# Optimization experiments

Measured on AMD Instinct MI355X. Metric: run time of the kernel, lower is better.

## Reference

```python
import jax, jax.numpy as jnp
import numpy as np

B, N, S, D = 32, 128, 64, 512
MAX_LEN = 5000


def make_pe(d_model, max_len):
    pos = np.arange(max_len, dtype=np.float32)[:, None]
    div = np.exp(np.arange(0, d_model, 2, dtype=np.float32) * (-np.log(10000.0) / d_model))
    pe = np.zeros((max_len, d_model), dtype=np.float32)
    pe[:, 0::2] = np.sin(pos * div)
    pe[:, 1::2] = np.cos(pos * div)
    return jnp.asarray(pe)


def setup_inputs() -> dict:
    key = jax.random.key(0)
    ks = jax.random.split(key, 16)
    s1 = 1.0 / np.sqrt(D)
    s2 = 1.0 / np.sqrt(2 * D)
    inp = {
        "x": jax.random.normal(ks[0], (B, N), jnp.float32),
        "timesteps": jax.random.randint(ks[1], (B,), 0, 1000),
        "fusion_feat": jax.random.normal(ks[2], (B, D), jnp.float32),
        "tar_image_feat": jax.random.normal(ks[3], (B, N, S, D), jnp.float32),
        "pe": make_pe(D, MAX_LEN),
        # torch Linear weights are [out, in]
        "Wq": jax.random.normal(ks[4], (D, D), jnp.float32) * s1,
        "Wk": jax.random.normal(ks[5], (D, D), jnp.float32) * s1,
        "Wv": jax.random.normal(ks[6], (D, D), jnp.float32) * s1,
        "Wp": jax.random.normal(ks[7], (D, D), jnp.float32) * s1,
        "bp": jnp.zeros((D,), jnp.float32),
        "Wt1": jax.random.normal(ks[8], (D, D), jnp.float32) * s1,
        "bt1": jnp.zeros((D,), jnp.float32),
        "Wt2": jax.random.normal(ks[9], (D, D), jnp.float32) * s1,
        "bt2": jnp.zeros((D,), jnp.float32),
        "Wd1": jax.random.normal(ks[10], (2 * D, 2 * D), jnp.float32) * s2,
        "bd1": jnp.zeros((2 * D,), jnp.float32),
        "Wd2": jax.random.normal(ks[11], (1, 2 * D), jnp.float32) * s2,
        "bd2": jnp.zeros((1,), jnp.float32),
    }
    return inp


def reference(x, timesteps, fusion_feat, tar_image_feat, pe,
              Wq, Wk, Wv, Wp, bp, Wt1, bt1, Wt2, bt2, Wd1, bd1, Wd2, bd2):
    # timestep embedding: pe[timesteps] -> [B, D], then 2-layer SiLU MLP (eval mode: dropout off)
    cond = jax.nn.silu(pe[timesteps] @ Wt1.T + bt1) @ Wt2.T + bt2  # [B, D]

    # similarity argmax over S tokens, then gather best token per (b, n)
    sim = jnp.einsum('bd,bnsd->bns', fusion_feat, tar_image_feat)  # [B, N, S]
    best = jnp.argmax(sim, axis=-1)                                # [B, N]
    tif = jnp.take_along_axis(tar_image_feat, best[:, :, None, None], axis=2)[:, :, 0, :]  # [B, N, D]

    # single-vector attention over N candidates
    q = (fusion_feat + cond) @ Wq.T                  # [B, D]
    k = (tif + cond[:, None, :]) @ Wk.T              # [B, N, D]
    v = (tif + cond[:, None, :]) @ Wv.T              # [B, N, D]
    w = jax.nn.softmax(jnp.einsum('bd,bnd->bn', q, k) + x, axis=-1)  # [B, N]
    new_emb = jnp.einsum('bn,bnd->bd', w, v) @ Wp.T + bp             # [B, D]

    # MLP decode over concat [new_emb (broadcast), tif]
    emb = jnp.concatenate([jnp.broadcast_to(new_emb[:, None, :], tif.shape), tif], axis=-1)  # [B, N, 2D]
    h = jax.nn.relu(emb @ Wd1.T + bd1)
    p = (h @ Wd2.T + bd2)[..., 0] + w                # [B, N]

    # sort descending along N
    return -jnp.sort(-p, axis=1)
```

## Files before the change

kernel.cpp:

```cpp
#include <hip/hip_runtime.h>
#include <hip/hip_bf16.h>
#include <math.h>


#define BB 32
#define NN 128
#define SS 64
#define DD 512

typedef __attribute__((ext_vector_type(8))) short short8;
typedef __attribute__((ext_vector_type(4))) float f32x4;

__device__ __forceinline__ ushort f2bf(float f) {
    unsigned u = __float_as_uint(f);
    unsigned r = (u + 0x7fffu + ((u >> 16) & 1u)) >> 16;
    return (ushort)r;
}

__device__ __forceinline__ void wave_dot512x4(
    const float* __restrict__ w, size_t ldw, float4 xa, float4 xb,
    int lane, float out[4]) {
    float4 ra[4], rb[4];
#pragma unroll
    for (int r = 0; r < 4; ++r) {
        const float4* row = reinterpret_cast<const float4*>(w + (size_t)r * ldw);
        ra[r] = row[lane * 2];
        rb[r] = row[lane * 2 + 1];
    }
#pragma unroll
    for (int r = 0; r < 4; ++r) {
        float s = ra[r].x * xa.x + ra[r].y * xa.y + ra[r].z * xa.z + ra[r].w * xa.w
                + rb[r].x * xb.x + rb[r].y * xb.y + rb[r].z * xb.z + rb[r].w * xb.w;
#pragma unroll
        for (int off = 32; off; off >>= 1) s += __shfl_xor(s, off);
        out[r] = s;
    }
}

__global__ __launch_bounds__(256) void bmv(
    const float* __restrict__ W, int ldw, const float* __restrict__ bias,
    const float* __restrict__ Xa, const float* __restrict__ Xb,
    const int* __restrict__ ts, const float* __restrict__ pe,
    float* __restrict__ Y, int R, int act, int mode) {
    __shared__ __align__(16) float xl[DD];
    int b = blockIdx.y, tid = threadIdx.x, lane = tid & 63, wave = tid >> 6;
    const float* src = (mode == 1) ? (pe + (size_t)ts[b] * DD) : (Xa + (size_t)b * DD);
    if (mode == 2) {
        const float* s2 = Xb + (size_t)b * DD;
        for (int i = tid; i < DD; i += 256) xl[i] = src[i] + s2[i];
    } else {
        for (int i = tid; i < DD; i += 256) xl[i] = src[i];
    }
    __syncthreads();
    float4 xa = reinterpret_cast<const float4*>(xl)[lane * 2];
    float4 xb = reinterpret_cast<const float4*>(xl)[lane * 2 + 1];
    int j0 = blockIdx.x * 16 + wave * 4;
    float s[4];
    wave_dot512x4(W + (size_t)j0 * ldw, ldw, xa, xb, lane, s);
    if (lane < 4) {
        int j = j0 + lane;
        float v = s[lane];
        if (bias) v += bias[j];
        if (act == 1) v = v / (1.f + expf(-v));
        Y[(size_t)b * R + j] = v;
    }
}

__global__ __launch_bounds__(256) void k_qk(
    const float* __restrict__ Wk, const float* __restrict__ q,
    float* __restrict__ qk) {
    __shared__ __align__(16) float ql[DD];
    __shared__ float part[4][64];
    int b = blockIdx.y, c0 = blockIdx.x * 64;
    int tid = threadIdx.x, lane = tid & 63, wave = tid >> 6;
    for (int i = tid; i < DD; i += 256) ql[i] = q[(size_t)b * DD + i];
    __syncthreads();
    float p = 0.f;
    for (int j = wave * 128; j < wave * 128 + 128; ++j)
        p += ql[j] * Wk[(size_t)j * DD + c0 + lane];
    part[wave][lane] = p;
    __syncthreads();
    if (tid < 64)
        qk[(size_t)b * DD + c0 + tid] =
            part[0][tid] + part[1][tid] + part[2][tid] + part[3][tid];
}

__global__ __launch_bounds__(256) void k2_sim(
    const float* __restrict__ fusion, const float* __restrict__ tif,
    const float* __restrict__ x, const float* __restrict__ qk,
    const float* __restrict__ Wd1, ushort* __restrict__ Wb,
    float* __restrict__ tif_best, ushort* __restrict__ abf,
    float* __restrict__ score) {
    __shared__ __align__(16) float fb[DD];
    __shared__ float bv_s[4];
    __shared__ int bi_s[4];
    __shared__ int bidx_s;
    __shared__ float dred[4];
    int bn = blockIdx.x, b = bn >> 7;
    int tid = threadIdx.x, lane = tid & 63, wave = tid >> 6;

    if (bn < 1024) {
        int idx = (bn * 256 + tid) * 2;
        int r = idx >> 9, k = idx & 511;
        float2 v = *reinterpret_cast<const float2*>(Wd1 + (size_t)r * 1024 + 512 + k);
        ushort2 o = {f2bf(v.x), f2bf(v.y)};
        *reinterpret_cast<ushort2*>(Wb + (size_t)r * 512 + k) = o;
    }

    for (int i = tid; i < DD; i += 256) fb[i] = fusion[(size_t)b * DD + i];
    __syncthreads();
    float4 xa = reinterpret_cast<const float4*>(fb)[lane * 2];
    float4 xb = reinterpret_cast<const float4*>(fb)[lane * 2 + 1];
    const float* base = tif + (size_t)bn * SS * DD;
    float bv = -INFINITY;
    int bi = 0;
    for (int s0 = wave * 16; s0 < wave * 16 + 16; s0 += 4) {
        float sv[4];
        wave_dot512x4(base + (size_t)s0 * DD, DD, xa, xb, lane, sv);
#pragma unroll
        for (int r = 0; r < 4; ++r)
            if (sv[r] > bv) { bv = sv[r]; bi = s0 + r; }
    }
    if (lane == 0) { bv_s[wave] = bv; bi_s[wave] = bi; }
    __syncthreads();
    if (tid == 0) {
        float v = bv_s[0]; int i0 = bi_s[0];
        for (int w = 1; w < 4; w++)
            if (bv_s[w] > v) { v = bv_s[w]; i0 = bi_s[w]; }
        bidx_s = i0;
    }
    __syncthreads();
    const float* src = base + (size_t)bidx_s * DD;
    const float* qkb = qk + (size_t)b * DD;
    float local = 0.f;
    for (int i = tid; i < DD; i += 256) {
        float vv = src[i];
        tif_best[(size_t)bn * DD + i] = vv;
        abf[(size_t)bn * DD + i] = f2bf(vv);
        local += vv * qkb[i];
    }
#pragma unroll
    for (int off = 32; off; off >>= 1) local += __shfl_xor(local, off);
    if (lane == 0) dred[wave] = local;
    __syncthreads();
    if (tid == 0) score[bn] = dred[0] + dred[1] + dred[2] + dred[3] + x[bn];
}

__global__ __launch_bounds__(256) void k_vsum(
    const float* __restrict__ score, const float* __restrict__ tif_best,
    const float* __restrict__ cond,
    float* __restrict__ wout, float* __restrict__ vsum) {
    __shared__ float wl[NN];
    __shared__ float redm[2], reds[2];
    int b = blockIdx.y, tid = threadIdx.x, lane = tid & 63, wave = tid >> 6;
    float v = 0.f;
    if (tid < NN) {
        v = score[b * NN + tid];
        float m = v;
#pragma unroll
        for (int off = 32; off; off >>= 1) m = fmaxf(m, __shfl_xor(m, off));
        if (lane == 0) redm[wave] = m;
    }
    __syncthreads();
    float m = fmaxf(redm[0], redm[1]);
    if (tid < NN) {
        float e = expf(v - m);
        wl[tid] = e;
        float s = e;
#pragma unroll
        for (int off = 32; off; off >>= 1) s += __shfl_xor(s, off);
        if (lane == 0) reds[wave] = s;
    }
    __syncthreads();
    float inv = 1.f / (reds[0] + reds[1]);
    if (blockIdx.x == 0 && tid < NN) wout[b * NN + tid] = wl[tid] * inv;
    int d = blockIdx.x * 256 + tid;
    const float* base = tif_best + (size_t)b * NN * DD + d;
    float s = 0.f;
#pragma unroll 8
    for (int n = 0; n < NN; n++) s += wl[n] * base[(size_t)n * DD];
    vsum[(size_t)b * DD + d] = s * inv + cond[(size_t)b * DD + d];
}

__global__ __launch_bounds__(256) void k4_mfma(
    const ushort* __restrict__ Abf, const ushort* __restrict__ Wb,
    const float* __restrict__ Wd1, const float* __restrict__ bd1,
    const float* __restrict__ ne, const float* __restrict__ Wd2,
    float* __restrict__ p_part) {
    __shared__ ushort aS[2][128 * 64];
    __shared__ ushort bS[2][128 * 64];
    __shared__ __align__(16) float nel[DD];
    __shared__ float uloc[128];
    int tid = threadIdx.x, l = tid & 63, w = tid >> 6;
    int m0 = blockIdx.x * 128, n0 = blockIdx.y * 128;
    int b = blockIdx.x;
    int wm = w >> 1, wn = w & 1;

    for (int i = tid; i < DD; i += 256) nel[i] = ne[(size_t)b * DD + i];
    __syncthreads();
    float4 na = reinterpret_cast<const float4*>(nel)[l * 2];
    float4 nb = reinterpret_cast<const float4*>(nel)[l * 2 + 1];

#define STAGE(K0, BUF)                                                         \
    {                                                                          \
        _Pragma("unroll") for (int i = 0; i < 4; ++i) {                        \
            int L = i * 4096 + w * 1024 + l * 16;                              \
            int row = L >> 7;                                                  \
            int bo = L & 127;                                                  \
            int sb = bo ^ ((row & 7) << 4);                                    \
            const ushort* ga = Abf + (size_t)(m0 + row) * DD + (K0) + (sb >> 1); \
            const ushort* gb = Wb + (size_t)(n0 + row) * DD + (K0) + (sb >> 1);  \
            __builtin_amdgcn_global_load_lds(                                  \
                (const __attribute__((address_space(1))) void*)ga,             \
                (__attribute__((address_space(3))) void*)(aS[BUF] + i * 2048 + w * 512), \
                16, 0, 0);                                                     \
            __builtin_amdgcn_global_load_lds(                                  \
                (const __attribute__((address_space(1))) void*)gb,             \
                (__attribute__((address_space(3))) void*)(bS[BUF] + i * 2048 + w * 512), \
                16, 0, 0);                                                     \
        }                                                                      \
    }

    STAGE(0, 0);
    for (int j0 = 0; j0 < 32; j0 += 4) {
        int r = w * 32 + j0;
        float s[4];
        wave_dot512x4(Wd1 + (size_t)(n0 + r) * 1024, 1024, na, nb, l, s);
        if (l < 4) uloc[r + l] = s[l] + bd1[n0 + r + l];
    }
    __syncthreads();

    f32x4 acc[4][4];
#pragma unroll
    for (int i = 0; i < 4; i++)
#pragma unroll
        for (int j = 0; j < 4; j++) acc[i][j] = (f32x4){0.f, 0.f, 0.f, 0.f};

    int cur = 0;
    for (int k0 = 0; k0 < DD; k0 += 64) {
        if (k0 + 64 < DD) STAGE(k0 + 64, cur ^ 1);
#pragma unroll
        for (int kk = 0; kk < 2; ++kk) {
            short8 af[4], bf[4];
#pragma unroll
            for (int f = 0; f < 4; ++f) {
                int ra = wm * 64 + f * 16 + (l & 15);
                int boa = (((l >> 4) * 16 + kk * 64)) ^ ((ra & 7) << 4);
                af[f] = *reinterpret_cast<const short8*>(&aS[cur][ra * 64 + (boa >> 1)]);
                int rb = wn * 64 + f * 16 + (l & 15);
                int bob = (((l >> 4) * 16 + kk * 64)) ^ ((rb & 7) << 4);
                bf[f] = *reinterpret_cast<const short8*>(&bS[cur][rb * 64 + (bob >> 1)]);
            }
#pragma unroll
            for (int fm = 0; fm < 4; ++fm)
#pragma unroll
                for (int fn = 0; fn < 4; ++fn)
                    acc[fm][fn] = __builtin_amdgcn_mfma_f32_16x16x32_bf16(
                        af[fm], bf[fn], acc[fm][fn], 0, 0, 0);
        }
        __syncthreads();
        cur ^= 1;
    }
#undef STAGE
#pragma unroll
    for (int fm = 0; fm < 4; ++fm) {
#pragma unroll
        for (int reg = 0; reg < 4; ++reg) {
            float pp = 0.f;
#pragma unroll
            for (int fn = 0; fn < 4; ++fn) {
                int rl = wn * 64 + fn * 16 + (l & 15);
                float hh = acc[fm][fn][reg] + uloc[rl];
                if (hh > 0.f) pp += Wd2[n0 + rl] * hh;
            }
#pragma unroll
            for (int off = 1; off < 16; off <<= 1) pp += __shfl_xor(pp, off);
            if ((l & 15) == 0) {
                int m = m0 + wm * 64 + fm * 16 + (l >> 4) * 4 + reg;
                p_part[(size_t)m * 16 + blockIdx.y * 2 + wn] = pp;
            }
        }
    }
}

__global__ __launch_bounds__(128) void k5_sort(
    const float* __restrict__ p_part, const float* __restrict__ wout,
    const float* __restrict__ bd2, float* __restrict__ out) {
    __shared__ float v[NN];
    int b = blockIdx.x, tid = threadIdx.x;
    int bn = b * NN + tid;
    float s = bd2[0] + wout[bn];
#pragma unroll
    for (int c = 0; c < 16; c++) s += p_part[(size_t)bn * 16 + c];
    v[tid] = s;
    __syncthreads();
    for (int k = 2; k <= NN; k <<= 1) {
        for (int j = k >> 1; j > 0; j >>= 1) {
            int ixj = tid ^ j;
            if (ixj > tid) {
                float a = v[tid], bb2 = v[ixj];
                bool desc = (tid & k) == 0;
                if (desc ? (a < bb2) : (a > bb2)) { v[tid] = bb2; v[ixj] = a; }
            }
            __syncthreads();
        }
    }
    out[bn] = v[tid];
}

extern "C" void kernel_launch(void* const* d_in, const int* in_sizes, int n_in,
                              void* d_out, int out_size, void* d_ws, size_t ws_size,
                              hipStream_t stream) {
    const float* x      = (const float*)d_in[0];
    const int*   ts     = (const int*)d_in[1];
    const float* fusion = (const float*)d_in[2];
    const float* tif    = (const float*)d_in[3];
    const float* pe     = (const float*)d_in[4];
    const float* Wq     = (const float*)d_in[5];
    const float* Wk     = (const float*)d_in[6];
    const float* Wv     = (const float*)d_in[7];
    const float* Wp     = (const float*)d_in[8];
    const float* bp     = (const float*)d_in[9];
    const float* Wt1    = (const float*)d_in[10];
    const float* bt1    = (const float*)d_in[11];
    const float* Wt2    = (const float*)d_in[12];
    const float* bt2    = (const float*)d_in[13];
    const float* Wd1    = (const float*)d_in[14];
    const float* bd1    = (const float*)d_in[15];
    const float* Wd2    = (const float*)d_in[16];
    const float* bd2    = (const float*)d_in[17];

    float* ws = (float*)d_ws;
    float* cond     = ws;
    float* qk       = cond + 16384;
    float* h        = qk + 16384;
    float* q        = h + 16384;
    float* score    = q + 16384;
    float* wout     = score + 4096;
    float* vsum     = wout + 4096;
    float* ve       = vsum + 16384;
    float* ne       = ve + 16384;
    float* p_part   = ne + 16384;
    float* tif_best = p_part + 65536;
    ushort* Abf     = (ushort*)(tif_best + 2097152);
    ushort* Wb      = Abf + 2097152;
    float* out = (float*)d_out;

    hipLaunchKernelGGL(bmv, dim3(32, BB), dim3(256), 0, stream,
                       Wt1, DD, bt1, nullptr, nullptr, ts, pe, h, DD, 1, 1);
    hipLaunchKernelGGL(bmv, dim3(32, BB), dim3(256), 0, stream,
                       Wt2, DD, bt2, h, nullptr, nullptr, nullptr, cond, DD, 0, 0);
    hipLaunchKernelGGL(bmv, dim3(32, BB), dim3(256), 0, stream,
                       Wq, DD, nullptr, fusion, cond, nullptr, nullptr, q, DD, 0, 2);
    hipLaunchKernelGGL(k_qk, dim3(8, BB), dim3(256), 0, stream, Wk, q, qk);

    hipLaunchKernelGGL(k2_sim, dim3(BB * NN), dim3(256), 0, stream,
                       fusion, tif, x, qk, Wd1, Wb, tif_best, Abf, score);

    hipLaunchKernelGGL(k_vsum, dim3(2, BB), dim3(256), 0, stream,
                       score, tif_best, cond, wout, vsum);
    hipLaunchKernelGGL(bmv, dim3(32, BB), dim3(256), 0, stream,
                       Wv, DD, nullptr, vsum, nullptr, nullptr, nullptr, ve, DD, 0, 0);
    hipLaunchKernelGGL(bmv, dim3(32, BB), dim3(256), 0, stream,
                       Wp, DD, bp, ve, nullptr, nullptr, nullptr, ne, DD, 0, 0);

    hipLaunchKernelGGL(k4_mfma, dim3(32, 8), dim3(256), 0, stream,
                       Abf, Wb, Wd1, bd1, ne, Wd2, p_part);
    hipLaunchKernelGGL(k5_sort, dim3(BB), dim3(128), 0, stream,
                       p_part, wout, bd2, out);
}
```

Baseline: 187.6 us.

## Fold Wp·Wv into one matrix, drop fp32 tif_best, move Wd1 cast

Precomputes Wpv = Wp·Wv with a tiled fp32 GEMM in 64 extra blocks of the similarity kernel, so the two chained matvecs (Wv then Wp) become one. Removes the fp32 tif_best buffer, and the weighted value sum now reads the bf16 copy of the best tokens, which lowers precision of that sum. Moves the Wd1 bf16 conversion into the first bmv launch. This cuts memory traffic and one launch, but adds a weight-weight GEMM on every call.

Result: slower. 195.8 us (+4.4%).

```diff
diff --git a/kernel.cpp b/kernel.cpp
--- a/kernel.cpp
+++ b/kernel.cpp
@@ -16,6 +16,9 @@
     unsigned r = (u + 0x7fffu + ((u >> 16) & 1u)) >> 16;
     return (ushort)r;
 }
+__device__ __forceinline__ float bf2f(ushort u) {
+    return __uint_as_float(((unsigned)u) << 16);
+}
 
 __device__ __forceinline__ void wave_dot512x4(
     const float* __restrict__ w, size_t ldw, float4 xa, float4 xb,
@@ -41,9 +44,17 @@
     const float* __restrict__ W, int ldw, const float* __restrict__ bias,
     const float* __restrict__ Xa, const float* __restrict__ Xb,
     const int* __restrict__ ts, const float* __restrict__ pe,
-    float* __restrict__ Y, int R, int act, int mode) {
+    float* __restrict__ Y, int R, int act, int mode,
+    const float* __restrict__ Wd1c, ushort* __restrict__ Wbc) {
     __shared__ __align__(16) float xl[DD];
     int b = blockIdx.y, tid = threadIdx.x, lane = tid & 63, wave = tid >> 6;
+    if (Wd1c) {
+        int idx = ((blockIdx.y * gridDim.x + blockIdx.x) * 256 + tid) * 2;
+        int r = idx >> 9, k = idx & 511;
+        float2 v = *reinterpret_cast<const float2*>(Wd1c + (size_t)r * 1024 + 512 + k);
+        ushort2 o = {f2bf(v.x), f2bf(v.y)};
+        *reinterpret_cast<ushort2*>(Wbc + (size_t)r * 512 + k) = o;
+    }
     const float* src = (mode == 1) ? (pe + (size_t)ts[b] * DD) : (Xa + (size_t)b * DD);
     if (mode == 2) {
         const float* s2 = Xb + (size_t)b * DD;
@@ -88,25 +99,64 @@
 __global__ __launch_bounds__(256) void k2_sim(
     const float* __restrict__ fusion, const float* __restrict__ tif,
     const float* __restrict__ x, const float* __restrict__ qk,
-    const float* __restrict__ Wd1, ushort* __restrict__ Wb,
-    float* __restrict__ tif_best, ushort* __restrict__ abf,
-    float* __restrict__ score) {
+    const float* __restrict__ Wp, const float* __restrict__ Wv,
+    float* __restrict__ Wpv,
+    ushort* __restrict__ abf, float* __restrict__ score) {
     __shared__ __align__(16) float fb[DD];
     __shared__ float bv_s[4];
     __shared__ int bi_s[4];
     __shared__ int bidx_s;
     __shared__ float dred[4];
-    int bn = blockIdx.x, b = bn >> 7;
+    __shared__ __align__(16) float wp_t[32][68];
+    __shared__ __align__(16) float wv_t[32][64];
+    int bn = blockIdx.x;
     int tid = threadIdx.x, lane = tid & 63, wave = tid >> 6;
 
-    if (bn < 1024) {
-        int idx = (bn * 256 + tid) * 2;
-        int r = idx >> 9, k = idx & 511;
-        float2 v = *reinterpret_cast<const float2*>(Wd1 + (size_t)r * 1024 + 512 + k);
-        ushort2 o = {f2bf(v.x), f2bf(v.y)};
-        *reinterpret_cast<ushort2*>(Wb + (size_t)r * 512 + k) = o;
-    }
-
+    if (bn >= BB * NN) {
+        int g = bn - BB * NN;
+        int i0 = (g & 7) * 64, d0 = (g >> 3) * 64;
+        int ti = (tid & 15) * 4, td = (tid >> 4) * 4;
+        float acc[4][4] = {};
+        for (int j0 = 0; j0 < DD; j0 += 32) {
+#pragma unroll
+            for (int q2 = 0; q2 < 2; ++q2) {
+                int s = tid * 2 + q2;
+                int i = s >> 3, j4 = (s & 7) * 4;
+                float4 v = *reinterpret_cast<const float4*>(
+                    Wp + (size_t)(i0 + i) * DD + j0 + j4);
+                wp_t[j4 + 0][i] = v.x; wp_t[j4 + 1][i] = v.y;
+                wp_t[j4 + 2][i] = v.z; wp_t[j4 + 3][i] = v.w;
+            }
+#pragma unroll
+            for (int q2 = 0; q2 < 2; ++q2) {
+                int s = tid * 2 + q2;
+                int j = s >> 4, d4 = (s & 15) * 4;
+                float4 v = *reinterpret_cast<const float4*>(
+                    Wv + (size_t)(j0 + j) * DD + d0 + d4);
+                *reinterpret_cast<float4*>(&wv_t[j][d4]) = v;
+            }
+            __syncthreads();
+#pragma unroll 8
+            for (int j = 0; j < 32; ++j) {
+                float4 a = *reinterpret_cast<const float4*>(&wp_t[j][ti]);
+                float4 bv = *reinterpret_cast<const float4*>(&wv_t[j][td]);
+                float a_[4] = {a.x, a.y, a.z, a.w};
+                float b_[4] = {bv.x, bv.y, bv.z, bv.w};
+#pragma unroll
+                for (int e = 0; e < 4; ++e)
+#pragma unroll
+                    for (int f = 0; f < 4; ++f) acc[e][f] += a_[e] * b_[f];
+            }
+            __syncthreads();
+        }
+#pragma unroll
+        for (int e = 0; e < 4; ++e)
+            *reinterpret_cast<float4*>(&Wpv[(size_t)(i0 + ti + e) * DD + d0 + td]) =
+                *reinterpret_cast<float4*>(acc[e]);
+        return;
+    }
+
+    int b = bn >> 7;
     for (int i = tid; i < DD; i += 256) fb[i] = fusion[(size_t)b * DD + i];
     __syncthreads();
     float4 xa = reinterpret_cast<const float4*>(fb)[lane * 2];
@@ -135,7 +185,6 @@
     float local = 0.f;
     for (int i = tid; i < DD; i += 256) {
         float vv = src[i];
-        tif_best[(size_t)bn * DD + i] = vv;
         abf[(size_t)bn * DD + i] = f2bf(vv);
         local += vv * qkb[i];
     }
@@ -147,7 +196,7 @@
 }
 
 __global__ __launch_bounds__(256) void k_vsum(
-    const float* __restrict__ score, const float* __restrict__ tif_best,
+    const float* __restrict__ score, const ushort* __restrict__ abf,
     const float* __restrict__ cond,
     float* __restrict__ wout, float* __restrict__ vsum) {
     __shared__ float wl[NN];
@@ -175,10 +224,10 @@
     float inv = 1.f / (reds[0] + reds[1]);
     if (blockIdx.x == 0 && tid < NN) wout[b * NN + tid] = wl[tid] * inv;
     int d = blockIdx.x * 256 + tid;
-    const float* base = tif_best + (size_t)b * NN * DD + d;
+    const ushort* base = abf + (size_t)b * NN * DD + d;
     float s = 0.f;
 #pragma unroll 8
-    for (int n = 0; n < NN; n++) s += wl[n] * base[(size_t)n * DD];
+    for (int n = 0; n < NN; n++) s += wl[n] * bf2f(base[(size_t)n * DD]);
     vsum[(size_t)b * DD + d] = s * inv + cond[(size_t)b * DD + d];
 }
 
@@ -338,31 +387,32 @@
     float* score    = q + 16384;
     float* wout     = score + 4096;
     float* vsum     = wout + 4096;
-    float* ve       = vsum + 16384;
-    float* ne       = ve + 16384;
-    float* p_part   = ne + 16384;
-    float* tif_best = p_part + 65536;
-    ushort* Abf     = (ushort*)(tif_best + 2097152);
+    float* ne       = vsum + 16384;
+    float* Wpv      = ne + 16384;
+    float* p_part   = Wpv + 262144;
+    ushort* Abf     = (ushort*)(p_part + 65536);
     ushort* Wb      = Abf + 2097152;
     float* out = (float*)d_out;
 
     hipLaunchKernelGGL(bmv, dim3(32, BB), dim3(256), 0, stream,
-                       Wt1, DD, bt1, nullptr, nullptr, ts, pe, h, DD, 1, 1);
+                       Wt1, DD, bt1, nullptr, nullptr, ts, pe, h, DD, 1, 1,
+                       Wd1, Wb);
     hipLaunchKernelGGL(bmv, dim3(32, BB), dim3(256), 0, stream,
-                       Wt2, DD, bt2, h, nullptr, nullptr, nullptr, cond, DD, 0, 0);
+                       Wt2, DD, bt2, h, nullptr, nullptr, nullptr, cond, DD, 0, 0,
+                       nullptr, nullptr);
     hipLaunchKernelGGL(bmv, dim3(32, BB), dim3(256), 0, stream,
-                       Wq, DD, nullptr, fusion, cond, nullptr, nullptr, q, DD, 0, 2);
+                       Wq, DD, nullptr, fusion, cond, nullptr, nullptr, q, DD, 0, 2,
+                       nullptr, nullptr);
     hipLaunchKernelGGL(k_qk, dim3(8, BB), dim3(256), 0, stream, Wk, q, qk);
 
-    hipLaunchKernelGGL(k2_sim, dim3(BB * NN), dim3(256), 0, stream,
-                       fusion, tif, x, qk, Wd1, Wb, tif_best, Abf, score);
+    hipLaunchKernelGGL(k2_sim, dim3(BB * NN + 64), dim3(256), 0, stream,
+                       fusion, tif, x, qk, Wp, Wv, Wpv, Abf, score);
 
     hipLaunchKernelGGL(k_vsum, dim3(2, BB), dim3(256), 0, stream,
-                       score, tif_best, cond, wout, vsum);
+                       score, Abf, cond, wout, vsum);
     hipLaunchKernelGGL(bmv, dim3(32, BB), dim3(256), 0, stream,
-                       Wv, DD, nullptr, vsum, nullptr, nullptr, nullptr, ve, DD, 0, 0);
-    hipLaunchKernelGGL(bmv, dim3(32, BB), dim3(256), 0, stream,
-                       Wp, DD, bp, ve, nullptr, nullptr, nullptr, ne, DD, 0, 0);
+                       Wpv, DD, bp, vsum, nullptr, nullptr, nullptr, ne, DD, 0, 0,
+                       nullptr, nullptr);
 
     hipLaunchKernelGGL(k4_mfma, dim3(32, 8), dim3(256), 0, stream,
                        Abf, Wb, Wd1, bd1, ne, Wd2, p_part);
```
